# Kernel tuning notes

Hardware: AMD Instinct MI355X
Metric: run time of the kernel (lower is better)

Reference implementation:

```python
import jax, jax.numpy as jnp
import numpy as np
import math

BATCH, LEN, HID, STATE = 16, 4096, 512, 128
DT_MIN, DT_MAX = 1e-3, 0.1
STEP_RESCALE = 1.0
CONJ_SYM = True


def setup_inputs() -> dict:
    key = jax.random.key(0)
    ks = jax.random.split(key, 7)
    inputs = jax.random.normal(ks[0], (BATCH, LEN, HID), jnp.float32)
    # stable continuous-time eigenvalues: negative real part
    lambda_real = -0.5 * jnp.abs(jax.random.normal(ks[1], (STATE,), jnp.float32)) - 1e-3
    lambda_imag = jnp.pi * jax.random.normal(ks[2], (STATE,), jnp.float32)
    B = jax.random.normal(ks[3], (STATE, HID, 2), jnp.float32) * (1.0 / math.sqrt(HID))
    C = jax.random.normal(ks[4], (HID, STATE, 2), jnp.float32) * (1.0 / math.sqrt(STATE))
    D = jax.random.normal(ks[5], (HID,), jnp.float32)
    u = jax.random.uniform(ks[6], (STATE, 1), jnp.float32)
    log_step = u * (math.log(DT_MAX) - math.log(DT_MIN)) + math.log(DT_MIN)
    return dict(inputs=inputs, lambda_real=lambda_real, lambda_imag=lambda_imag,
                B=B, C=C, D=D, log_step=log_step)


def _s5_forward(inputs, lambda_real, lambda_imag, B, C, D, log_step):
    # complex diagonal state matrix (P,)
    lam = (lambda_real + 1j * lambda_imag).astype(jnp.complex64)
    step = STEP_RESCALE * jnp.exp(log_step[:, 0])          # (P,)
    lambda_bar = jnp.exp(lam * step.astype(jnp.complex64))  # ZOH discretization, (P,)
    B_c = (B[..., 0] + 1j * B[..., 1]).astype(jnp.complex64)  # (P, H)
    C_c = (C[..., 0] + 1j * C[..., 1]).astype(jnp.complex64)  # (H, P)
    # ZOH input matrix: B_bar = (lambda_bar - 1) / lambda * B
    b_bar = ((lambda_bar - 1.0) / lam)[:, None] * B_c          # (P, H)
    # per-timestep driving term: (L, B, P)
    bu = jnp.einsum('blh,ph->lbp', inputs.astype(jnp.complex64), b_bar)
    L = inputs.shape[1]
    a = jnp.broadcast_to(lambda_bar[None, None, :], (L, 1, STATE))  # constant decay per step

    def combine(e1, e2):
        a1, b1 = e1
        a2, b2 = e2
        return (a2 * a1, a2 * b1 + b2)

    # parallel (Blelchoch-style) scan of x_t = lambda_bar * x_{t-1} + bu_t
    _, states = jax.lax.associative_scan(combine, (a, bu))      # states: (L, B, P)
    y = jnp.einsum('lbp,hp->blh', states, C_c)                  # (B, L, H) complex
    out = 2.0 * y.real if CONJ_SYM else y.real
    return out + D * inputs


def reference(inputs, lambda_real, lambda_imag, B, C, D, log_step):
    return _s5_forward(inputs, lambda_real, lambda_imag, B, C, D, log_step)
```

## Files before the change

kernel.cpp:

```cpp
#include <hip/hip_runtime.h>
#include <math.h>

#define B_   16
#define L_   4096
#define H_   512
#define P_   128
#define M_   (B_*L_)
#define N2_  (2*P_)
#define CHK  64
#define NCH  (L_/CHK)

typedef __attribute__((ext_vector_type(8))) short bf16x8;
typedef __attribute__((ext_vector_type(8))) unsigned short u16x8;
typedef __attribute__((ext_vector_type(4))) float f32x4;
typedef __attribute__((ext_vector_type(4))) unsigned u32x4;

__device__ __forceinline__ unsigned short f2bf(float x) {
    unsigned u = __float_as_uint(x);
    return (unsigned short)((u + 0x7FFFu + ((u >> 16) & 1u)) >> 16);
}
__device__ __forceinline__ float bf2f(unsigned short s) {
    return __uint_as_float(((unsigned)s) << 16);
}
__device__ __forceinline__ unsigned cvtpk(float lo, float hi) {
    unsigned r;
    asm("v_cvt_pk_bf16_f32 %0, %1, %2" : "=v"(r) : "v"(lo), "v"(hi));
    return r;
}

__device__ __forceinline__ void gload16(const void* g, void* l) {
    __builtin_amdgcn_global_load_lds(
        (const __attribute__((address_space(1))) void*)g,
        (__attribute__((address_space(3))) void*)l,
        16, 0, 0);
}


__global__ void precompA(const float* __restrict__ lr, const float* __restrict__ li,
                         const float* __restrict__ lstep,
                         float* __restrict__ abar_r, float* __restrict__ abar_i,
                         float* __restrict__ coef_r, float* __restrict__ coef_i) {
    int p = threadIdx.x;
    if (p >= P_) return;
    double lrd = (double)lr[p], lid = (double)li[p];
    double step = exp((double)lstep[p]);
    double ea = exp(lrd * step);
    double abr = ea * cos(lid * step), abi = ea * sin(lid * step);
    abar_r[p] = (float)abr; abar_i[p] = (float)abi;
    double nr = abr - 1.0, ni = abi;
    double den = lrd*lrd + lid*lid;
    coef_r[p] = (float)((nr*lrd + ni*lid) / den);
    coef_i[p] = (float)((ni*lrd - nr*lid) / den);
}

__global__ void precompBT(const float* __restrict__ Bin,
                          const float* __restrict__ coef_r, const float* __restrict__ coef_i,
                          unsigned short* __restrict__ BTh) {
    int idx = blockIdx.x * 256 + threadIdx.x;
    if (idx >= N2_*H_) return;
    int n = idx >> 9, k = idx & 511;
    int p = n & (P_-1);
    float br = Bin[(p*H_ + k)*2 + 0], bi = Bin[(p*H_ + k)*2 + 1];
    float cr = coef_r[p], ci = coef_i[p];
    float v = (n < P_) ? (cr*br - ci*bi) : (cr*bi + ci*br);
    BTh[idx] = f2bf(v);
}

__global__ void precompCM(const float* __restrict__ Cin,
                          unsigned short* __restrict__ CMh) {
    int idx = blockIdx.x * 256 + threadIdx.x;
    if (idx >= H_*N2_) return;
    int n = idx >> 8, k = idx & 255;
    float v;
    if (k < P_) v =  2.0f * Cin[(n*P_ + k)*2 + 0];
    else        v = -2.0f * Cin[(n*P_ + (k-P_))*2 + 1];
    CMh[idx] = f2bf(v);
}


template<int KSTEPS>
__global__ __launch_bounds__(512) void gemm1f(
        const float* __restrict__ A,
        const unsigned short* __restrict__ Bm,
        unsigned short* __restrict__ bu) {
    constexpr int K = KSTEPS * 64;
    __shared__ float Asf[128 * 64];
    __shared__ unsigned short Bs[256 * 64];

    int t = threadIdx.x;
    int g = blockIdx.x;
    int nid = (g & 7) * (gridDim.x >> 3) + (g >> 3);
    int m0 = nid * 128;

    int lane = t & 63;
    int w    = t >> 6;
    int wr = w >> 2, wc = w & 3;
    int lr = lane & 15, lg = lane >> 4;

    int ar_ = t >> 4;
    int asw = (t & 15) ^ (ar_ & 15);
    const float* gA = A + (size_t)(m0 + ar_) * K + asw * 4;
    int br_ = t >> 3;
    int bsw = (t & 7) ^ (br_ & 7);
    const unsigned short* gB = Bm + (size_t)br_ * K + bsw * 8;

    f32x4 acc[4][4] = {};

    for (int ks = 0; ks < KSTEPS; ++ks) {
        int k0 = ks * 64;
        __syncthreads();
#pragma unroll
        for (int i = 0; i < 4; ++i)
            gload16(gA + (size_t)(32 * i) * K + k0, &Asf[i * 2048 + w * 256]);
#pragma unroll
        for (int i = 0; i < 4; ++i)
            gload16(gB + (size_t)(64 * i) * K + k0, &Bs[i * 4096 + w * 512]);
        __syncthreads();

#pragma unroll
        for (int ku = 0; ku < 2; ++ku) {
            bf16x8 af[4], bf[4];
#pragma unroll
            for (int f = 0; f < 4; ++f) {
                int rA = wr * 64 + f * 16 + lr;
                int c0 = ((ku * 8 + lg * 2)     ^ rA) & 15;
                int c1 = ((ku * 8 + lg * 2 + 1) ^ rA) & 15;
                float4 a0 = *(const float4*)&Asf[rA * 64 + c0 * 4];
                float4 a1 = *(const float4*)&Asf[rA * 64 + c1 * 4];
                u32x4 q;
                q[0] = cvtpk(a0.x, a0.y);
                q[1] = cvtpk(a0.z, a0.w);
                q[2] = cvtpk(a1.x, a1.y);
                q[3] = cvtpk(a1.z, a1.w);
                af[f] = *(bf16x8*)&q;
                int rB = wc * 64 + f * 16 + lr;
                int cb = ((ku * 4 + lg) ^ rB) & 7;
                bf[f] = *(const bf16x8*)&Bs[rB * 64 + cb * 8];
            }
#pragma unroll
            for (int fn = 0; fn < 4; ++fn)
#pragma unroll
                for (int fm = 0; fm < 4; ++fm)
                    acc[fn][fm] = __builtin_amdgcn_mfma_f32_16x16x32_bf16(bf[fn], af[fm], acc[fn][fm], 0, 0, 0);
        }
    }

#pragma unroll
    for (int fn = 0; fn < 4; ++fn)
#pragma unroll
        for (int fm = 0; fm < 4; ++fm) {
            int m = m0 + wr * 64 + fm * 16 + lr;
            int n = wc * 64 + fn * 16 + lg * 4;
            unsigned o0 = cvtpk(acc[fn][fm][0], acc[fn][fm][1]);
            unsigned o1 = cvtpk(acc[fn][fm][2], acc[fn][fm][3]);
            *(uint2*)&bu[(size_t)m * N2_ + n] = make_uint2(o0, o1);
        }
}


template<int KSTEPS, bool HASD>
__global__ __launch_bounds__(256) void gemm_m97(
        const unsigned short* __restrict__ A,
        const unsigned short* __restrict__ Bm,
        float* __restrict__ Cout, int N,
        const float* __restrict__ Din, const float* __restrict__ Dv) {
    constexpr int K = KSTEPS * 64;
    __shared__ unsigned short As[128 * 64];
    __shared__ unsigned short Bs[128 * 64];

    int t = threadIdx.x;
    int nx = gridDim.x;
    int flat = blockIdx.x + nx * blockIdx.y;
    int per  = (nx * gridDim.y) >> 3;
    int nid  = (flat & 7) * per + (flat >> 3);
    int n0 = (nid & (nx - 1)) * 128;
    int m0 = (nid / nx) * 128;

    int lane = t & 63;
    int w    = t >> 6;
    int wr = w >> 1, wc = w & 1;
    int lr = lane & 15, lg = lane >> 4;

    int sr_ = t >> 3;
    int ssw = (t & 7) ^ (sr_ & 7);
    const unsigned short* gA = A  + (size_t)(m0 + sr_) * K + ssw * 8;
    const unsigned short* gB = Bm + (size_t)(n0 + sr_) * K + ssw * 8;

    f32x4 acc[4][4] = {};

    for (int ks = 0; ks < KSTEPS; ++ks) {
        int k0 = ks * 64;
        __syncthreads();
#pragma unroll
        for (int i = 0; i < 4; ++i) {
            gload16(gA + (size_t)(32 * i) * K + k0, &As[i * 2048 + w * 512]);
            gload16(gB + (size_t)(32 * i) * K + k0, &Bs[i * 2048 + w * 512]);
        }
        __syncthreads();

#pragma unroll
        for (int ku = 0; ku < 2; ++ku) {
            bf16x8 af[4], bf[4];
#pragma unroll
            for (int f = 0; f < 4; ++f) {
                int rA = wr * 64 + f * 16 + lr;
                int ca = ((ku * 4 + lg) ^ rA) & 7;
                af[f] = *(const bf16x8*)&As[rA * 64 + ca * 8];
                int rB = wc * 64 + f * 16 + lr;
                int cb = ((ku * 4 + lg) ^ rB) & 7;
                bf[f] = *(const bf16x8*)&Bs[rB * 64 + cb * 8];
            }
#pragma unroll
            for (int fn = 0; fn < 4; ++fn)
#pragma unroll
                for (int fm = 0; fm < 4; ++fm)
                    acc[fn][fm] = __builtin_amdgcn_mfma_f32_16x16x32_bf16(bf[fn], af[fm], acc[fn][fm], 0, 0, 0);
        }
    }

#pragma unroll
    for (int fn = 0; fn < 4; ++fn)
#pragma unroll
        for (int fm = 0; fm < 4; ++fm) {
            int m = m0 + wr * 64 + fm * 16 + lr;
            int n = n0 + wc * 64 + fn * 16 + lg * 4;
            float4 v = make_float4(acc[fn][fm][0], acc[fn][fm][1], acc[fn][fm][2], acc[fn][fm][3]);
            if (HASD) {
                float4 di = *(const float4*)&Din[(size_t)m * N + n];
                float4 dv = *(const float4*)&Dv[n];
                v.x += dv.x * di.x; v.y += dv.y * di.y;
                v.z += dv.z * di.z; v.w += dv.w * di.w;
            }
            *(float4*)&Cout[(size_t)m * N + n] = v;
        }
}


__global__ __launch_bounds__(256) void scan_carry(const unsigned short* __restrict__ bu,
        const float* __restrict__ ar_, const float* __restrict__ ai_,
        float* __restrict__ carr) {
    __shared__ float lds[CHK][256];
    int t = threadIdx.x;
    int c = blockIdx.x, b = blockIdx.y;
    size_t base = ((size_t)(b*L_ + c*CHK)) * N2_;
    const unsigned short* g = bu + base;
#pragma unroll
    for (int it = 0; it < 8; it++) {
        int flat = it * 2048 + t * 8;
        u16x8 v = *(const u16x8*)&g[flat];
        float4 x0 = make_float4(bf2f(v[0]), bf2f(v[1]), bf2f(v[2]), bf2f(v[3]));
        float4 x1 = make_float4(bf2f(v[4]), bf2f(v[5]), bf2f(v[6]), bf2f(v[7]));
        *(float4*)&lds[0][flat]     = x0;
        *(float4*)&lds[0][flat + 4] = x1;
    }
    __syncthreads();
    if (t < 128) {
        float ar = ar_[t], ai = ai_[t];
        float xr = 0.f, xi = 0.f;
        for (int i = 0; i < CHK; i++) {
            float br = lds[i][t], bi = lds[i][t + 128];
            float nr = ar*xr - ai*xi + br;
            float ni = ar*xi + ai*xr + bi;
            xr = nr; xi = ni;
        }
        size_t o = ((size_t)(b*NCH + c)) * N2_;
        carr[o + t] = xr; carr[o + t + 128] = xi;
    }
}

__global__ void scan_chunks(const float* __restrict__ carr, float* __restrict__ pre,
                            const float* __restrict__ ar_, const float* __restrict__ ai_) {
    int id = blockIdx.x * 256 + threadIdx.x;
    if (id >= B_ * P_) return;
    int b = id >> 7, p = id & (P_-1);
    float mr = ar_[p], mi = ai_[p];
#pragma unroll
    for (int s = 0; s < 6; s++) { float tr = mr*mr - mi*mi; mi = 2.f*mr*mi; mr = tr; }
    float xr = 0.f, xi = 0.f;
    for (int c = 0; c < NCH; c++) {
        size_t o = ((size_t)(b*NCH + c)) * N2_;
        pre[o + p] = xr; pre[o + p + 128] = xi;
        float cr = carr[o + p], ci = carr[o + p + 128];
        float nr = mr*xr - mi*xi + cr;
        float ni = mr*xi + mi*xr + ci;
        xr = nr; xi = ni;
    }
}

__global__ __launch_bounds__(256) void scan_apply(const unsigned short* __restrict__ bu,
        const float* __restrict__ ar_, const float* __restrict__ ai_,
        const float* __restrict__ pre, unsigned short* __restrict__ states_h) {
    __shared__ float lds[CHK][256];
    int t = threadIdx.x;
    int c = blockIdx.x, b = blockIdx.y;
    size_t base = ((size_t)(b*L_ + c*CHK)) * N2_;
    const unsigned short* g = bu + base;
#pragma unroll
    for (int it = 0; it < 8; it++) {
        int flat = it * 2048 + t * 8;
        u16x8 v = *(const u16x8*)&g[flat];
        float4 x0 = make_float4(bf2f(v[0]), bf2f(v[1]), bf2f(v[2]), bf2f(v[3]));
        float4 x1 = make_float4(bf2f(v[4]), bf2f(v[5]), bf2f(v[6]), bf2f(v[7]));
        *(float4*)&lds[0][flat]     = x0;
        *(float4*)&lds[0][flat + 4] = x1;
    }
    __syncthreads();
    if (t < 128) {
        float ar = ar_[t], ai = ai_[t];
        size_t o = ((size_t)(b*NCH + c)) * N2_;
        float xr = pre[o + t], xi = pre[o + t + 128];
        for (int i = 0; i < CHK; i++) {
            float br = lds[i][t], bi = lds[i][t + 128];
            float nr = ar*xr - ai*xi + br;
            float ni = ar*xi + ai*xr + bi;
            xr = nr; xi = ni;
            lds[i][t] = xr; lds[i][t + 128] = xi;
        }
    }
    __syncthreads();
    unsigned short* o = states_h + base;
#pragma unroll
    for (int it = 0; it < 8; it++) {
        int flat = it * 2048 + t * 8;
        float4 v0 = *(const float4*)&lds[0][flat];
        float4 v1 = *(const float4*)&lds[0][flat + 4];
        unsigned q0 = cvtpk(v0.x, v0.y);
        unsigned q1 = cvtpk(v0.z, v0.w);
        unsigned q2 = cvtpk(v1.x, v1.y);
        unsigned q3 = cvtpk(v1.z, v1.w);
        u32x4 q = {q0, q1, q2, q3};
        *(u32x4*)&o[flat] = q;
    }
}


extern "C" void kernel_launch(void* const* d_in, const int* in_sizes, int n_in,
                              void* d_out, int out_size, void* d_ws, size_t ws_size,
                              hipStream_t stream) {
    const float* inputs = (const float*)d_in[0];
    const float* lr     = (const float*)d_in[1];
    const float* li     = (const float*)d_in[2];
    const float* Bin    = (const float*)d_in[3];
    const float* Cin    = (const float*)d_in[4];
    const float* Dv     = (const float*)d_in[5];
    const float* lstep  = (const float*)d_in[6];
    float* out = (float*)d_out;

    unsigned short* bu = (unsigned short*)d_out;

    float* ws     = (float*)d_ws;
    float* abar_r = ws;
    float* abar_i = ws + 128;
    float* coef_r = ws + 256;
    float* coef_i = ws + 384;
    float* carr   = ws + 512;
    float* pre    = ws + 262656;
    unsigned short* BTh = (unsigned short*)(ws + 524800);
    unsigned short* CMh = BTh + N2_*H_;
    unsigned short* states_h = CMh + H_*N2_;

    hipLaunchKernelGGL(precompA, dim3(1), dim3(128), 0, stream,
                       lr, li, lstep, abar_r, abar_i, coef_r, coef_i);
    hipLaunchKernelGGL(precompBT, dim3((N2_*H_)/256), dim3(256), 0, stream,
                       Bin, coef_r, coef_i, BTh);
    hipLaunchKernelGGL(precompCM, dim3((H_*N2_)/256), dim3(256), 0, stream,
                       Cin, CMh);
    hipLaunchKernelGGL((gemm1f<8>), dim3(M_/128), dim3(512), 0, stream,
                       inputs, BTh, bu);
    hipLaunchKernelGGL(scan_carry, dim3(NCH, B_), dim3(256), 0, stream,
                       bu, abar_r, abar_i, carr);
    hipLaunchKernelGGL(scan_chunks, dim3((B_*P_)/256), dim3(256), 0, stream,
                       carr, pre, abar_r, abar_i);
    hipLaunchKernelGGL(scan_apply, dim3(NCH, B_), dim3(256), 0, stream,
                       bu, abar_r, abar_i, pre, states_h);
    hipLaunchKernelGGL((gemm_m97<4, true>), dim3(H_/128, M_/128), dim3(256), 0, stream,
                       states_h, CMh, out, H_, inputs, Dv);
}
```

Measured before the change: 138.0 us.

## Fuse chunk-carry scan into bu GEMM epilogue via LDS tile

Measured after the change: 147.3 us. +6.7%, slower.

```diff
diff --git a/kernel.cpp b/kernel.cpp
--- a/kernel.cpp
+++ b/kernel.cpp
@@ -82,10 +82,14 @@
 __global__ __launch_bounds__(512) void gemm1f(
         const float* __restrict__ A,
         const unsigned short* __restrict__ Bm,
-        unsigned short* __restrict__ bu) {
+        unsigned short* __restrict__ bu,
+        const float* __restrict__ abr_, const float* __restrict__ abi_,
+        float* __restrict__ carr) {
     constexpr int K = KSTEPS * 64;
-    __shared__ float Asf[128 * 64];
-    __shared__ unsigned short Bs[256 * 64];
+    __shared__ unsigned long long smem[8192];
+    float*          Asf = (float*)smem;
+    unsigned short* Bs  = (unsigned short*)(smem + 4096);
+    unsigned short* Tile= (unsigned short*)smem;
 
     int t = threadIdx.x;
     int g = blockIdx.x;
@@ -145,16 +149,46 @@
         }
     }
 
+    __syncthreads();
+
 #pragma unroll
     for (int fn = 0; fn < 4; ++fn)
 #pragma unroll
         for (int fm = 0; fm < 4; ++fm) {
-            int m = m0 + wr * 64 + fm * 16 + lr;
+            int m = wr * 64 + fm * 16 + lr;
             int n = wc * 64 + fn * 16 + lg * 4;
             unsigned o0 = cvtpk(acc[fn][fm][0], acc[fn][fm][1]);
             unsigned o1 = cvtpk(acc[fn][fm][2], acc[fn][fm][3]);
-            *(uint2*)&bu[(size_t)m * N2_ + n] = make_uint2(o0, o1);
-        }
+            *(uint2*)&bu[(size_t)(m0 + m) * N2_ + n] = make_uint2(o0, o1);
+            int cs = ((n >> 3) ^ (m & 7));
+            *(uint2*)&Tile[m * 256 + cs * 8 + (n & 7)] = make_uint2(o0, o1);
+        }
+    __syncthreads();
+
+    if (t < P_) {
+        int p = t;
+        float ar = abr_[p], ai = abi_[p];
+        int b   = m0 >> 12;
+        int c64 = (m0 & (L_-1)) >> 6;
+        float xr = 0.f, xi = 0.f;
+        int ch0 = p >> 3, ch1 = (p + 128) >> 3;
+#pragma unroll 16
+        for (int i = 0; i < 128; ++i) {
+            int sw = i & 7;
+            float brr = bf2f(Tile[i * 256 + ((ch0 ^ sw) << 3) + (p & 7)]);
+            float bii = bf2f(Tile[i * 256 + ((ch1 ^ sw) << 3) + (p & 7)]);
+            float nr = ar * xr - ai * xi + brr;
+            float ni = ar * xi + ai * xr + bii;
+            xr = nr; xi = ni;
+            if (i == 63) {
+                size_t o = ((size_t)(b * NCH + c64)) * N2_;
+                carr[o + p] = xr; carr[o + p + 128] = xi;
+                xr = 0.f; xi = 0.f;
+            }
+        }
+        size_t o = ((size_t)(b * NCH + c64 + 1)) * N2_;
+        carr[o + p] = xr; carr[o + p + 128] = xi;
+    }
 }
 
 
@@ -236,38 +270,6 @@
 }
 
 
-__global__ __launch_bounds__(256) void scan_carry(const unsigned short* __restrict__ bu,
-        const float* __restrict__ ar_, const float* __restrict__ ai_,
-        float* __restrict__ carr) {
-    __shared__ float lds[CHK][256];
-    int t = threadIdx.x;
-    int c = blockIdx.x, b = blockIdx.y;
-    size_t base = ((size_t)(b*L_ + c*CHK)) * N2_;
-    const unsigned short* g = bu + base;
-#pragma unroll
-    for (int it = 0; it < 8; it++) {
-        int flat = it * 2048 + t * 8;
-        u16x8 v = *(const u16x8*)&g[flat];
-        float4 x0 = make_float4(bf2f(v[0]), bf2f(v[1]), bf2f(v[2]), bf2f(v[3]));
-        float4 x1 = make_float4(bf2f(v[4]), bf2f(v[5]), bf2f(v[6]), bf2f(v[7]));
-        *(float4*)&lds[0][flat]     = x0;
-        *(float4*)&lds[0][flat + 4] = x1;
-    }
-    __syncthreads();
-    if (t < 128) {
-        float ar = ar_[t], ai = ai_[t];
-        float xr = 0.f, xi = 0.f;
-        for (int i = 0; i < CHK; i++) {
-            float br = lds[i][t], bi = lds[i][t + 128];
-            float nr = ar*xr - ai*xi + br;
-            float ni = ar*xi + ai*xr + bi;
-            xr = nr; xi = ni;
-        }
-        size_t o = ((size_t)(b*NCH + c)) * N2_;
-        carr[o + t] = xr; carr[o + t + 128] = xi;
-    }
-}
-
 __global__ void scan_chunks(const float* __restrict__ carr, float* __restrict__ pre,
                             const float* __restrict__ ar_, const float* __restrict__ ai_) {
     int id = blockIdx.x * 256 + threadIdx.x;
@@ -366,9 +368,7 @@
     hipLaunchKernelGGL(precompCM, dim3((H_*N2_)/256), dim3(256), 0, stream,
                        Cin, CMh);
     hipLaunchKernelGGL((gemm1f<8>), dim3(M_/128), dim3(512), 0, stream,
-                       inputs, BTh, bu);
-    hipLaunchKernelGGL(scan_carry, dim3(NCH, B_), dim3(256), 0, stream,
-                       bu, abar_r, abar_i, carr);
+                       inputs, BTh, bu, abar_r, abar_i, carr);
     hipLaunchKernelGGL(scan_chunks, dim3((B_*P_)/256), dim3(256), 0, stream,
                        carr, pre, abar_r, abar_i);
     hipLaunchKernelGGL(scan_apply, dim3(NCH, B_), dim3(256), 0, stream,
```
